# Optimization experiments

Hardware: AMD Instinct MI355X
Metric: run time of the kernel (lower is better)

## Reference

```python
import jax, jax.numpy as jnp
import numpy as np

NX, NY = 4096, 4096
T = 1.0
TIME_STEPS = 400
DT = T / TIME_STEPS
DX = 1.0 / (NX - 1)
DY = 1.0 / (NY - 1)
Z = 1.0
FROG = 2
BC = jnp.array([-1.0, 1.0], dtype=jnp.float32)


def _conv_ax0(A, f):
    # valid cross-correlation along axis 0 (matches F.conv1d after transpose)
    L = f.shape[0]
    n = A.shape[0] - L + 1
    out = f[0] * A[0:n, :]
    for k in range(1, L):
        out = out + f[k] * A[k:k + n, :]
    return out


def _conv_ax1(A, f):
    L = f.shape[0]
    n = A.shape[1] - L + 1
    out = f[0] * A[:, 0:n]
    for k in range(1, L):
        out = out + f[k] * A[:, k:k + n]
    return out


def _amper(E, Hx, Hy, f, s):
    # S1: d/dx of Hy ; S2: d/dy of Hx
    S1 = (Z * DT / DX) * _conv_ax0(Hy, f)[0:-1, s:NY - s]
    S2 = (Z * DT / DY) * _conv_ax1(Hx, f)[s:NX - s, 0:-1]
    return E[s:NX - s, s:NY - s] + S1 - S2


def _faraday(E, Hx, Hy, f, s):
    S3 = (DT / (Z * DY)) * _conv_ax1(E, f)[s:NX - s, :]
    S4 = (DT / (Z * DX)) * _conv_ax0(E, f)[:, s:NY - s]
    Ax = Hx[s:NX - s, s - 1:NY - s] - S3
    Ay = Hy[s - 1:NX - s, s:NY - s] + S4
    return Ax, Ay


def setup_inputs() -> dict:
    key = jax.random.key(0)
    k1, k2, k3 = jax.random.split(key, 3)
    X1 = jax.random.normal(k1, (NX, NY), dtype=jnp.float32)
    X2 = jax.random.normal(k2, (NX, NY), dtype=jnp.float32)
    X3 = jax.random.normal(k3, (NX, NY), dtype=jnp.float32)
    w1 = jnp.ones((1,), dtype=jnp.float32)
    return {"X1": X1, "X2": X2, "X3": X3, "w1": w1}


def reference(X1, X2, X3, w1):
    f4 = jnp.concatenate([(w1 - 1.0) / 3.0, -w1, w1, (1.0 - w1) / 3.0])
    E, Hx, Hy = X1, X2, X3
    # boundary-order then interior (frog) Ampere update of E
    E = E.at[1:NX - 1, 1:NY - 1].set(_amper(X1, X2, X3, BC, 1))
    E = E.at[FROG:NX - FROG, FROG:NY - FROG].set(_amper(E, X2, X3, f4, FROG))
    # Faraday updates of Hx, Hy from the ORIGINAL fields (bc order)
    Ax1, Ay1 = _faraday(X1, X2, X3, BC, 1)
    Hx = Hx.at[1:NX - 1, 0:NY - 1].set(Ax1)
    Hy = Hy.at[0:NX - 1, 1:NY - 1].set(Ay1)
    # interior Faraday updates using updated E, Hx, Hy
    Ax2, Ay2 = _faraday(E, Hx, Hy, f4, FROG)
    Hx = Hx.at[FROG:NX - FROG, FROG - 1:NY - FROG].set(Ax2)
    Hy = Hy.at[FROG - 1:NX - FROG, FROG:NY - FROG].set(Ay2)
    return (E, Hx, Hy)
```

## Files before the change

### kernel.cpp

```cpp
#include <hip/hip_runtime.h>

#define NXg 4096
#define NYg 4096
#define RPT 8
#define ROW0 8
#define NBANDS 510
#define BTHREADS 128

static constexpr float C = 10.2375f;

struct F7  { float v[7];  };
struct F10 { float v[10]; };

__device__ __forceinline__ void ld12(const float* __restrict__ P, int r, int c0,
                                     float4& a, float4& b, float4& c) {
    const size_t o = (size_t)r * NYg + c0;
    a = *(const float4*)(P + o - 4);
    b = *(const float4*)(P + o);
    c = *(const float4*)(P + o + 4);
}

__device__ __forceinline__ F7 mk7(const float4& a, const float4& b, const float4& c) {
    F7 r;
    r.v[0] = a.w; r.v[1] = b.x; r.v[2] = b.y; r.v[3] = b.z;
    r.v[4] = b.w; r.v[5] = c.x; r.v[6] = c.y;
    return r;
}
__device__ __forceinline__ F10 mk10(const float4& a, const float4& b, const float4& c) {
    F10 r;
    r.v[0] = a.y; r.v[1] = a.z; r.v[2] = a.w;
    r.v[3] = b.x; r.v[4] = b.y; r.v[5] = b.z; r.v[6] = b.w;
    r.v[7] = c.x; r.v[8] = c.y; r.v[9] = c.z;
    return r;
}

__device__ __forceinline__ F7 ld7(const float* __restrict__ P, int r, int c0) {
    float4 a, b, c; ld12(P, r, c0, a, b, c); return mk7(a, b, c);
}
__device__ __forceinline__ F10 ld10(const float* __restrict__ P, int r, int c0) {
    float4 a, b, c; ld12(P, r, c0, a, b, c); return mk10(a, b, c);
}

__global__ __launch_bounds__(BTHREADS, 2) void fat_kernel(
    const float* __restrict__ X1, const float* __restrict__ X2,
    const float* __restrict__ X3, const float* __restrict__ w1,
    float* __restrict__ E, float* __restrict__ Hx, float* __restrict__ Hy)
{
    const int t  = threadIdx.x;
    const int c0 = (blockIdx.x * BTHREADS + t) * 4;
    const int i0 = ROW0 + blockIdx.y * RPT;
    const bool gL = (c0 == 0);
    const bool gR = (c0 == NYg - 4);

    const float wv = w1[0];
    const float f0 = (wv - 1.0f) / 3.0f;
    const float f1 = -wv;
    const float f2 = wv;
    const float f3 = (1.0f - wv) / 3.0f;

    auto eRow = [&](const F7& x3m2, const F7& x3m1, const F7& x3p0, const F7& x3p1,
                    const F10& x2r, const F7& x1r) -> F7 {
        F7 e;
        #pragma unroll
        for (int m = 0; m < 7; ++m) {
            const float e1 = x1r.v[m] + C * (x3p0.v[m] - x3m1.v[m])
                                      - C * (x2r.v[m + 2] - x2r.v[m + 1]);
            e.v[m] = e1
                + C * (f0 * x3m2.v[m] + f1 * x3m1.v[m] + f2 * x3p0.v[m] + f3 * x3p1.v[m])
                - C * (f0 * x2r.v[m] + f1 * x2r.v[m + 1] + f2 * x2r.v[m + 2] + f3 * x2r.v[m + 3]);
        }
        if (gL) {
            e.v[1] = x1r.v[1];
            e.v[2] = x1r.v[2] + C * (x3p0.v[2] - x3m1.v[2])
                              - C * (x2r.v[4] - x2r.v[3]);
        }
        if (gR) {
            e.v[4] = x1r.v[4];
            e.v[3] = x1r.v[3] + C * (x3p0.v[3] - x3m1.v[3])
                              - C * (x2r.v[5] - x2r.v[4]);
        }
        return e;
    };

    F7 p3a = ld7(X3, i0 - 3, c0);
    F7 p3b = ld7(X3, i0 - 2, c0);
    F7 p3c = ld7(X3, i0 - 1, c0);
    F7 w3[4];
    w3[0] = ld7(X3, i0,     c0);
    w3[1] = ld7(X3, i0 + 1, c0);
    w3[2] = ld7(X3, i0 + 2, c0);
    w3[3] = ld7(X3, i0 + 3, c0);

    F10 q2a = ld10(X2, i0 - 1, c0);
    F10 q2b = ld10(X2, i0,     c0);
    F10 q2c = ld10(X2, i0 + 1, c0);
    F10 w2r = ld10(X2, i0 + 2, c0);

    F7 q1a = ld7(X1, i0 - 1, c0);
    F7 w1r[3];
    w1r[0] = ld7(X1, i0,     c0);
    w1r[1] = ld7(X1, i0 + 1, c0);
    w1r[2] = ld7(X1, i0 + 2, c0);

    F7 ew[4];
    ew[0] = eRow(p3a, p3b, p3c, w3[0], q2a, q1a);
    ew[1] = eRow(p3b, p3c, w3[0], w3[1], q2b, w1r[0]);
    ew[2] = eRow(p3c, w3[0], w3[1], w3[2], q2c, w1r[1]);

    float x2c0[4] = {q2b.v[3], q2b.v[4], q2b.v[5], q2b.v[6]};
    float x2c1[4] = {q2c.v[3], q2c.v[4], q2c.v[5], q2c.v[6]};

    #pragma unroll
    for (int s = 0; s < RPT; ++s) {
        const int i = i0 + s;

        F7  t3; F10 t2; F7 t1;
        if (s < RPT - 1) {
            t3 = ld7(X3, i + 4, c0);
            t2 = ld10(X2, i + 3, c0);
            t1 = ld7(X1, i + 3, c0);
        }

        ew[3] = eRow(w3[0], w3[1], w3[2], w3[3], w2r, w1r[2]);

        float hx[4], hy[4];
        #pragma unroll
        for (int q = 0; q < 4; ++q) {
            hx[q] = x2c0[q] - C * (w1r[0].v[q + 2] - w1r[0].v[q + 1])
                  - C * (f0 * ew[1].v[q]     + f1 * ew[1].v[q + 1]
                       + f2 * ew[1].v[q + 2] + f3 * ew[1].v[q + 3]);
            hy[q] = w3[0].v[q + 1] + C * (w1r[1].v[q + 1] - w1r[0].v[q + 1])
                  + C * (f0 * ew[0].v[q + 1] + f1 * ew[1].v[q + 1]
                       + f2 * ew[2].v[q + 1] + f3 * ew[3].v[q + 1]);
        }
        if (gL) {
            hx[0] = x2c0[0] - C * (w1r[0].v[2] - w1r[0].v[1]);
            hy[0] = w3[0].v[1];
            hy[1] = w3[0].v[2] + C * (w1r[1].v[2] - w1r[0].v[2]);
        }
        if (gR) {
            hx[3] = x2c0[3];
            hy[3] = w3[0].v[4];
            hx[2] = x2c0[2] - C * (w1r[0].v[4] - w1r[0].v[3]);
            hy[2] = w3[0].v[3] + C * (w1r[1].v[3] - w1r[0].v[3]);
        }

        const size_t idx = (size_t)i * NYg + c0;
        *(float4*)(E  + idx) = make_float4(ew[1].v[1], ew[1].v[2], ew[1].v[3], ew[1].v[4]);
        *(float4*)(Hx + idx) = make_float4(hx[0], hx[1], hx[2], hx[3]);
        *(float4*)(Hy + idx) = make_float4(hy[0], hy[1], hy[2], hy[3]);

        ew[0] = ew[1]; ew[1] = ew[2]; ew[2] = ew[3];
        w3[0] = w3[1]; w3[1] = w3[2]; w3[2] = w3[3];
        w1r[0] = w1r[1]; w1r[1] = w1r[2];
        #pragma unroll
        for (int q = 0; q < 4; ++q) { x2c0[q] = x2c1[q]; x2c1[q] = w2r.v[3 + q]; }
        if (s < RPT - 1) { w3[3] = t3; w2r = t2; w1r[2] = t1; }
    }
}

#define TRE 8
#define EROWSE 12
#define ECOLSE 136

__global__ __launch_bounds__(256) void edge_kernel(
    const float* __restrict__ X1, const float* __restrict__ X2,
    const float* __restrict__ X3, const float* __restrict__ w1,
    float* __restrict__ E, float* __restrict__ Hx, float* __restrict__ Hy)
{
    __shared__ float elds[EROWSE][ECOLSE];
    const int t    = threadIdx.x;
    const int row0 = blockIdx.y ? (NXg - TRE) : 0;
    const int col0 = blockIdx.x * 128;

    const float wv = w1[0];
    const float f0 = (wv - 1.0f) / 3.0f;
    const float f1 = -wv;
    const float f2 = wv;
    const float f3 = (1.0f - wv) / 3.0f;

    for (int cidx = t; cidx < EROWSE * ECOLSE; cidx += 256) {
        const int r  = cidx / ECOLSE;
        const int cc = cidx - r * ECOLSE;
        const int gr = row0 - 2 + r;
        const int gc = col0 - 4 + cc;
        float e = 0.0f;
        if (gr >= 0 && gr < NXg && gc >= 0 && gc < NYg) {
            const size_t idx = (size_t)gr * NYg + gc;
            const float x1 = X1[idx];
            if (gr == 0 || gr == NXg - 1 || gc == 0 || gc == NYg - 1) {
                e = x1;
            } else {
                float e1 = x1 + C * (X3[idx] - X3[idx - NYg])
                              - C * (X2[idx] - X2[idx - 1]);
                if (gr >= 2 && gr <= NXg - 3 && gc >= 2 && gc <= NYg - 3) {
                    e1 += C * (f0 * X3[idx - 2 * NYg] + f1 * X3[idx - NYg]
                             + f2 * X3[idx] + f3 * X3[idx + NYg])
                        - C * (f0 * X2[idx - 2] + f1 * X2[idx - 1]
                             + f2 * X2[idx] + f3 * X2[idx + 1]);
                }
                e = e1;
            }
        }
        elds[r][cc] = e;
    }
    __syncthreads();

    for (int cidx = t; cidx < TRE * 128; cidx += 256) {
        const int hr  = cidx >> 7;
        const int tc  = cidx & 127;
        const int gr  = row0 + hr;
        const int gcc = col0 + tc;
        const size_t idx = (size_t)gr * NYg + gcc;
        const int lr  = hr + 2;
        const int lc2 = tc + 4;

        const float ec = elds[lr][lc2];
        E[idx] = ec;

        const float x1 = X1[idx];

        float hx = X2[idx];
        if (gr >= 1 && gr <= NXg - 2 && gcc <= NYg - 2)
            hx -= C * (X1[idx + 1] - x1);
        if (gr >= 2 && gr <= NXg - 3 && gcc >= 1 && gcc <= NYg - 3) {
            hx -= C * (f0 * elds[lr][lc2 - 1] + f1 * ec
                     + f2 * elds[lr][lc2 + 1] + f3 * elds[lr][lc2 + 2]);
        }
        Hx[idx] = hx;

        float hy = X3[idx];
        if (gr <= NXg - 2 && gcc >= 1 && gcc <= NYg - 2)
            hy += C * (X1[idx + NYg] - x1);
        if (gr >= 1 && gr <= NXg - 3 && gcc >= 2 && gcc <= NYg - 3) {
            hy += C * (f0 * elds[lr - 1][lc2] + f1 * ec
                     + f2 * elds[lr + 1][lc2] + f3 * elds[lr + 2][lc2]);
        }
        Hy[idx] = hy;
    }
}

extern "C" void kernel_launch(void* const* d_in, const int* in_sizes, int n_in,
                              void* d_out, int out_size, void* d_ws, size_t ws_size,
                              hipStream_t stream) {
    const float* X1 = (const float*)d_in[0];
    const float* X2 = (const float*)d_in[1];
    const float* X3 = (const float*)d_in[2];
    const float* w1 = (const float*)d_in[3];

    float* E  = (float*)d_out;
    float* Hx = (float*)d_out + (size_t)NXg * NYg;
    float* Hy = (float*)d_out + 2 * (size_t)NXg * NYg;

    edge_kernel<<<dim3(32, 2), 256, 0, stream>>>(X1, X2, X3, w1, E, Hx, Hy);
    fat_kernel <<<dim3(NYg / (BTHREADS * 4), NBANDS), BTHREADS, 0, stream>>>(
        X1, X2, X3, w1, E, Hx, Hy);
}
```

Measured before the change: 105.4 us.

## Stage input halo tiles into LDS via async global_load_lds before compute

The fused stencil kernel now copies each block's 8-row band of X1/X2/X3 (with halos) into shared memory using the direct global-to-LDS load instruction, then computes from LDS. Work is split so each block covers a 256-column panel and each of two waves handles four rows, instead of one thread walking eight rows with register prefetch. The aim is to remove redundant overlapping float4 global loads and their latency. In exchange it adds a barrier, about 38 KB of LDS per block, and shorter per-thread row reuse (four rows), so more halo rows are re-read per output.

```diff
diff --git a/kernel.cpp b/kernel.cpp
--- a/kernel.cpp
+++ b/kernel.cpp
@@ -2,23 +2,20 @@
 
 #define NXg 4096
 #define NYg 4096
-#define RPT 8
+#define BROWS 8
 #define ROW0 8
 #define NBANDS 510
-#define BTHREADS 128
+#define NPANEL 16
+#define CCOLS 256
+#define LCOLS 264
+#define R3 14
+#define R2 11
+#define R1 11
 
 static constexpr float C = 10.2375f;
 
 struct F7  { float v[7];  };
 struct F10 { float v[10]; };
-
-__device__ __forceinline__ void ld12(const float* __restrict__ P, int r, int c0,
-                                     float4& a, float4& b, float4& c) {
-    const size_t o = (size_t)r * NYg + c0;
-    a = *(const float4*)(P + o - 4);
-    b = *(const float4*)(P + o);
-    c = *(const float4*)(P + o + 4);
-}
 
 __device__ __forceinline__ F7 mk7(const float4& a, const float4& b, const float4& c) {
     F7 r;
@@ -33,24 +30,62 @@
     r.v[7] = c.x; r.v[8] = c.y; r.v[9] = c.z;
     return r;
 }
-
-__device__ __forceinline__ F7 ld7(const float* __restrict__ P, int r, int c0) {
-    float4 a, b, c; ld12(P, r, c0, a, b, c); return mk7(a, b, c);
-}
-__device__ __forceinline__ F10 ld10(const float* __restrict__ P, int r, int c0) {
-    float4 a, b, c; ld12(P, r, c0, a, b, c); return mk10(a, b, c);
-}
-
-__global__ __launch_bounds__(BTHREADS, 2) void fat_kernel(
+__device__ __forceinline__ F7 l7(const float* Lrow, int lc) {
+    const float4 a = *(const float4*)(Lrow + lc - 4);
+    const float4 b = *(const float4*)(Lrow + lc);
+    const float4 c = *(const float4*)(Lrow + lc + 4);
+    return mk7(a, b, c);
+}
+__device__ __forceinline__ F10 l10(const float* Lrow, int lc) {
+    const float4 a = *(const float4*)(Lrow + lc - 4);
+    const float4 b = *(const float4*)(Lrow + lc);
+    const float4 c = *(const float4*)(Lrow + lc + 4);
+    return mk10(a, b, c);
+}
+
+__device__ __forceinline__ void gload_lds16(const float* g, float* l) {
+    __builtin_amdgcn_global_load_lds(
+        (const __attribute__((address_space(1))) void*)g,
+        (__attribute__((address_space(3))) void*)l, 16, 0, 0);
+}
+
+__global__ __launch_bounds__(128, 2) void band_kernel(
     const float* __restrict__ X1, const float* __restrict__ X2,
     const float* __restrict__ X3, const float* __restrict__ w1,
     float* __restrict__ E, float* __restrict__ Hx, float* __restrict__ Hy)
 {
-    const int t  = threadIdx.x;
-    const int c0 = (blockIdx.x * BTHREADS + t) * 4;
-    const int i0 = ROW0 + blockIdx.y * RPT;
-    const bool gL = (c0 == 0);
-    const bool gR = (c0 == NYg - 4);
+    __shared__ float L3[R3][LCOLS];
+    __shared__ float L2[R2][LCOLS];
+    __shared__ float L1[R1][LCOLS];
+
+    const int i0   = ROW0 + blockIdx.y * BROWS;
+    const int col0 = blockIdx.x * CCOLS;
+    const int wid  = threadIdx.x >> 6;
+    const int lane = threadIdx.x & 63;
+
+    for (int q = wid; q < 2 * (R3 + R2 + R1); q += 2) {
+        const int part = q & 1;
+        const int rid  = q >> 1;
+        const float* src;
+        float* lrow;
+        int grow;
+        if (rid < R3)           { src = X3; lrow = &L3[rid][0];           grow = i0 - 3 + rid; }
+        else if (rid < R3 + R2) { src = X2; lrow = &L2[rid - R3][0];      grow = i0 - 1 + (rid - R3); }
+        else                    { src = X1; lrow = &L1[rid - R3 - R2][0]; grow = i0 - 1 + (rid - R3 - R2); }
+        const float* g = src + (size_t)grow * NYg + (col0 - 4 + part * 8) + lane * 4;
+        gload_lds16(g, lrow + part * 8);
+    }
+    __syncthreads();
+
+    const int cq = threadIdx.x & 63;
+    const int g  = threadIdx.x >> 6;
+    const int lc = 4 + 4 * cq;
+    const int rb = 4 * g;
+    const int b3 = rb + 3;
+    const int b2 = rb + 1;
+
+    const bool gL = (blockIdx.x == 0) && (cq == 0);
+    const bool gR = (blockIdx.x == NPANEL - 1) && (cq == 63);
 
     const float wv = w1[0];
     const float f0 = (wv - 1.0f) / 3.0f;
@@ -82,25 +117,25 @@
         return e;
     };
 
-    F7 p3a = ld7(X3, i0 - 3, c0);
-    F7 p3b = ld7(X3, i0 - 2, c0);
-    F7 p3c = ld7(X3, i0 - 1, c0);
+    F7 p3a = l7(&L3[b3 - 3][0], lc);
+    F7 p3b = l7(&L3[b3 - 2][0], lc);
+    F7 p3c = l7(&L3[b3 - 1][0], lc);
     F7 w3[4];
-    w3[0] = ld7(X3, i0,     c0);
-    w3[1] = ld7(X3, i0 + 1, c0);
-    w3[2] = ld7(X3, i0 + 2, c0);
-    w3[3] = ld7(X3, i0 + 3, c0);
-
-    F10 q2a = ld10(X2, i0 - 1, c0);
-    F10 q2b = ld10(X2, i0,     c0);
-    F10 q2c = ld10(X2, i0 + 1, c0);
-    F10 w2r = ld10(X2, i0 + 2, c0);
-
-    F7 q1a = ld7(X1, i0 - 1, c0);
+    w3[0] = l7(&L3[b3][0],     lc);
+    w3[1] = l7(&L3[b3 + 1][0], lc);
+    w3[2] = l7(&L3[b3 + 2][0], lc);
+    w3[3] = l7(&L3[b3 + 3][0], lc);
+
+    F10 q2a = l10(&L2[b2 - 1][0], lc);
+    F10 q2b = l10(&L2[b2][0],     lc);
+    F10 q2c = l10(&L2[b2 + 1][0], lc);
+    F10 w2r = l10(&L2[b2 + 2][0], lc);
+
+    F7 q1a = l7(&L1[b2 - 1][0], lc);
     F7 w1r[3];
-    w1r[0] = ld7(X1, i0,     c0);
-    w1r[1] = ld7(X1, i0 + 1, c0);
-    w1r[2] = ld7(X1, i0 + 2, c0);
+    w1r[0] = l7(&L1[b2][0],     lc);
+    w1r[1] = l7(&L1[b2 + 1][0], lc);
+    w1r[2] = l7(&L1[b2 + 2][0], lc);
 
     F7 ew[4];
     ew[0] = eRow(p3a, p3b, p3c, w3[0], q2a, q1a);
@@ -111,15 +146,8 @@
     float x2c1[4] = {q2c.v[3], q2c.v[4], q2c.v[5], q2c.v[6]};
 
     #pragma unroll
-    for (int s = 0; s < RPT; ++s) {
-        const int i = i0 + s;
-
-        F7  t3; F10 t2; F7 t1;
-        if (s < RPT - 1) {
-            t3 = ld7(X3, i + 4, c0);
-            t2 = ld10(X2, i + 3, c0);
-            t1 = ld7(X1, i + 3, c0);
-        }
+    for (int s = 0; s < 4; ++s) {
+        const int i = i0 + rb + s;
 
         ew[3] = eRow(w3[0], w3[1], w3[2], w3[3], w2r, w1r[2]);
 
@@ -145,7 +173,7 @@
             hy[2] = w3[0].v[3] + C * (w1r[1].v[3] - w1r[0].v[3]);
         }
 
-        const size_t idx = (size_t)i * NYg + c0;
+        const size_t idx = (size_t)i * NYg + col0 + 4 * cq;
         *(float4*)(E  + idx) = make_float4(ew[1].v[1], ew[1].v[2], ew[1].v[3], ew[1].v[4]);
         *(float4*)(Hx + idx) = make_float4(hx[0], hx[1], hx[2], hx[3]);
         *(float4*)(Hy + idx) = make_float4(hy[0], hy[1], hy[2], hy[3]);
@@ -155,7 +183,11 @@
         w1r[0] = w1r[1]; w1r[1] = w1r[2];
         #pragma unroll
         for (int q = 0; q < 4; ++q) { x2c0[q] = x2c1[q]; x2c1[q] = w2r.v[3 + q]; }
-        if (s < RPT - 1) { w3[3] = t3; w2r = t2; w1r[2] = t1; }
+        if (s < 3) {
+            w3[3]  = l7 (&L3[b3 + 4 + s][0], lc);
+            w2r    = l10(&L2[b2 + 3 + s][0], lc);
+            w1r[2] = l7 (&L1[b2 + 3 + s][0], lc);
+        }
     }
 }
 
@@ -253,6 +285,5 @@
     float* Hy = (float*)d_out + 2 * (size_t)NXg * NYg;
 
     edge_kernel<<<dim3(32, 2), 256, 0, stream>>>(X1, X2, X3, w1, E, Hx, Hy);
-    fat_kernel <<<dim3(NYg / (BTHREADS * 4), NBANDS), BTHREADS, 0, stream>>>(
-        X1, X2, X3, w1, E, Hx, Hy);
-}
+    band_kernel<<<dim3(NPANEL, NBANDS), 128, 0, stream>>>(X1, X2, X3, w1, E, Hx, Hy);
+}
```

After: 98.04 us. -7.0%, faster.
